# Kernel tuning notes

Hardware: AMD Instinct MI355X
Metric: run time of the kernel (lower is better)

## Reference

```python
import jax, jax.numpy as jnp
import numpy as np
from jax import lax

EPS = 1e-10

def _ln(x, g, b):
    m = x.mean(-1, keepdims=True)
    v = x.var(-1, keepdims=True)
    return (x - m) / jnp.sqrt(v + 1e-5) * g + b

def _gather(t, idx):
    # t: (B, HW, c), idx: (B, HW, d) -> (B, HW, d, c); out[n,i,k,:] = t[n, idx[n,i,k], :]
    return jax.vmap(lambda tn, In: tn[In])(t, idx)

def setup_inputs() -> dict:
    key = jax.random.key(0)
    ks = jax.random.split(key, 20)
    b, v, c, d, h, w, hid, ksz = 2, 2, 128, 64, 64, 64, 256, 5
    hw = h * w
    Bf = b * v  # v_1 == 1 target view per reference view
    std = 0.02
    return {
        'features_mv': jax.random.normal(ks[0], (b, v, c, h, w), jnp.float32),
        'warp_indices': jax.random.randint(ks[1], (Bf, hw, d), 0, hw, jnp.int32),
        'depth_prob': jax.random.uniform(ks[2], (Bf, hw, d), jnp.float32),
        'ln1_g': jnp.ones((c,), jnp.float32), 'ln1_b': jnp.zeros((c,), jnp.float32),
        'wq': jax.random.normal(ks[3], (c, c), jnp.float32) * std, 'bq': jnp.zeros((c,), jnp.float32),
        'wk': jax.random.normal(ks[4], (c, c), jnp.float32) * std, 'bk': jnp.zeros((c,), jnp.float32),
        'wv': jax.random.normal(ks[5], (c, c), jnp.float32) * std, 'bv': jnp.zeros((c,), jnp.float32),
        'k_pe': jax.random.normal(ks[6], (1, 1, d), jnp.float32) * std,
        'v_pe': jax.random.normal(ks[7], (1, 1, d), jnp.float32) * std,
        'rpe': jax.random.normal(ks[8], (1, 1, d), jnp.float32) * std,
        'proj_w': jax.random.normal(ks[9], (c, c), jnp.float32) * std, 'proj_b': jnp.zeros((c,), jnp.float32),
        'ln2_g': jnp.ones((c,), jnp.float32), 'ln2_b': jnp.zeros((c,), jnp.float32),
        'fc1_w': jax.random.normal(ks[10], (c, hid), jnp.float32) * std, 'fc1_b': jnp.zeros((hid,), jnp.float32),
        'dw_w': jax.random.normal(ks[11], (hid, 1, ksz, ksz), jnp.float32) * std, 'dw_b': jnp.zeros((hid,), jnp.float32),
        'fc2_w': jax.random.normal(ks[12], (hid, c), jnp.float32) * std, 'fc2_b': jnp.zeros((c,), jnp.float32),
    }

def reference(features_mv, warp_indices, depth_prob, ln1_g, ln1_b, wq, bq, wk, bk, wv, bv,
              k_pe, v_pe, rpe, proj_w, proj_b, ln2_g, ln2_b, fc1_w, fc1_b, dw_w, dw_b, fc2_w, fc2_b):
    b, v, c, h, w = features_mv.shape
    hw = h * w
    hid = fc1_w.shape[1]
    scale = c ** (-0.5)  # num_heads = 1 -> head_dim = dim

    # (b v) (h w) c
    x = features_mv.reshape(b * v, c, hw).transpose(0, 2, 1)
    shortcut = x
    xn = _ln(x, ln1_g, ln1_b)
    q = xn @ wq + bq
    k = xn @ wk + bk
    vv = xn @ wv + bv

    # nn pairing: v=2, v_1=1 -> each reference view attends the other view
    Q = (q.reshape(b, v, hw, c) * scale).reshape(b * v, hw, c)
    K = k.reshape(b, v, hw, c)[:, ::-1].reshape(b * v, hw, c)
    V = vv.reshape(b, v, hw, c)[:, ::-1].reshape(b * v, hw, c)

    # SMM_QmK: cost[n,i,k] = sum_c Q[n,i,c] * K[n, idx[n,i,k], c]
    Kg = _gather(K, warp_indices)                       # (B, hw, d, c)
    cost = jnp.einsum('bic,bikc->bik', Q, Kg)
    Q_pe = Q.sum(-1, keepdims=True)                     # (B, hw, 1)
    cost = cost + Q_pe * k_pe + rpe                     # broadcast (1,1,d)

    # (Sim_UNet similarity refinement omitted: UNetModel source unavailable; identity here)
    attn = jax.nn.softmax(cost, axis=-1)
    attn = attn * depth_prob
    attn = (attn + EPS) / (attn.sum(-1, keepdims=True) + EPS)

    # SMM_AmV: out[n,i,c] = sum_k attn[n,i,k] * V[n, idx[n,i,k], c]
    Vg = _gather(V, warp_indices)                       # (B, hw, d, c)
    out = jnp.einsum('bik,bikc->bic', attn, Vg)
    out = out + (attn * v_pe).sum(-1, keepdims=True)

    # projection + residual (v_1 == 1 so B == b*v)
    x = shortcut + (out @ proj_w + proj_b)

    # ConvFFN residual branch
    xn2 = _ln(x, ln2_g, ln2_b)
    y = jax.nn.gelu(xn2 @ fc1_w + fc1_b, approximate=False)
    yi = y.transpose(0, 2, 1).reshape(b * v, hid, h, w)
    yc = lax.conv_general_dilated(yi, dw_w, (1, 1), 'SAME', feature_group_count=hid,
                                  dimension_numbers=('NCHW', 'OIHW', 'NCHW'))
    yc = jax.nn.gelu(yc + dw_b[None, :, None, None], approximate=False)
    y = y + yc.reshape(b * v, hid, hw).transpose(0, 2, 1)
    y = y @ fc2_w + fc2_b
    return x + y
```

## Files before the change

kernel.cpp:

```cpp
#include <hip/hip_runtime.h>
#include <math.h>

#define TOK   16384
#define HW    4096
#define C     128
#define D     64
#define HID   256

constexpr float LN_EPS = 1e-5f;
constexpr float EPS_R  = 1e-10f;
constexpr float QSCALE = 0.08838834764831845f;

typedef __attribute__((ext_vector_type(8))) short  bf16x8;
typedef __attribute__((ext_vector_type(4))) float  f32x4;
typedef __attribute__((ext_vector_type(2))) _Float16 half2v;
#define MFMA16(a, b, c) __builtin_amdgcn_mfma_f32_16x16x32_bf16((a), (b), (c), 0, 0, 0)

__device__ __forceinline__ float bflo(unsigned u) { return __uint_as_float(u << 16); }
__device__ __forceinline__ float bfhi(unsigned u) { return __uint_as_float(u & 0xffff0000u); }
__device__ __forceinline__ unsigned short f2bf(float f) {
  unsigned u = __float_as_uint(f);
  unsigned r = (u + 0x7fffu + ((u >> 16) & 1u)) >> 16;
  return (unsigned short)r;
}
__device__ __forceinline__ unsigned short f2h(float f) {
  _Float16 h = (_Float16)f;
  unsigned short r;
  __builtin_memcpy(&r, &h, 2);
  return r;
}
__device__ __forceinline__ float gelu_exact(float x) {
  return 0.5f * x * (1.0f + erff(x * 0.7071067811865476f));
}

union U4H { uint4 v; half2v h[4]; };
union U1H { unsigned v; half2v h; };

#if __has_builtin(__builtin_amdgcn_fdot2)
__device__ __forceinline__ float dot2h(half2v a, half2v b, float c) {
  return __builtin_amdgcn_fdot2(a, b, c, false);
}
#else
__device__ __forceinline__ float dot2h(half2v a, half2v b, float c) {
  return c + (float)a.x * (float)b.x + (float)a.y * (float)b.y;
}
#endif

__global__ __launch_bounds__(256) void k_prep(const float* __restrict__ wq,
    const float* __restrict__ wk, const float* __restrict__ wv,
    const float* __restrict__ pw, const float* __restrict__ f1w,
    const float* __restrict__ f2w, unsigned short* __restrict__ wt) {
  int id = blockIdx.x * 256 + threadIdx.x;
  if (id < 16384) {
    int n = id >> 7, k = id & 127;
    wt[id] = f2bf(wq[k * 128 + n]);
  } else if (id < 32768) {
    int e = id - 16384; int n = e >> 7, k = e & 127;
    wt[id] = f2bf(wk[k * 128 + n]);
  } else if (id < 49152) {
    int e = id - 32768; int n = e >> 7, k = e & 127;
    wt[id] = f2bf(wv[k * 128 + n]);
  } else if (id < 65536) {
    int e = id - 49152; int n = e >> 7, k = e & 127;
    wt[id] = f2bf(pw[k * 128 + n]);
  } else if (id < 98304) {
    int e = id - 65536; int n = e >> 7, k = e & 127;
    wt[id] = f2bf(f1w[k * 256 + n]);
  } else {
    int e = id - 98304; int n = e >> 8, k = e & 255;
    wt[id] = f2bf(f2w[k * 128 + n]);
  }
}

__global__ __launch_bounds__(256) void k_ln1qkv(const float* __restrict__ feat,
    const float* __restrict__ g, const float* __restrict__ b,
    const unsigned short* __restrict__ wt,
    const float* __restrict__ bq, const float* __restrict__ bk,
    const float* __restrict__ bv, unsigned short* __restrict__ qh,
    unsigned short* __restrict__ ksw, unsigned short* __restrict__ vsw) {
  __shared__ float t16[16][C + 1];
  __shared__ unsigned short axn[16 * C];
  int tid = threadIdx.x;
  int lane = tid & 63, wave = tid >> 6;
  int t0 = blockIdx.x * 16;
  int nv = t0 >> 12, i0 = t0 & 4095;
  const float* fb = feat + (size_t)nv * C * HW;
  for (int e = tid; e < 16 * C; e += 256) {
    int ch = e >> 4, ii = e & 15;
    t16[ii][ch] = fb[(size_t)ch * HW + i0 + ii];
  }
  __syncthreads();
  for (int tkn = wave; tkn < 16; tkn += 4) {
    float a0 = t16[tkn][lane];
    float a1 = t16[tkn][lane + 64];
    float s = a0 + a1;
    for (int off = 32; off; off >>= 1) s += __shfl_xor(s, off, 64);
    float mean = s * (1.0f / 128.0f);
    float d0 = a0 - mean, d1 = a1 - mean;
    float v = d0 * d0 + d1 * d1;
    for (int off = 32; off; off >>= 1) v += __shfl_xor(v, off, 64);
    float rstd = rsqrtf(v * (1.0f / 128.0f) + LN_EPS);
    unsigned short x0 = f2bf(d0 * rstd * g[lane] + b[lane]);
    unsigned short x1 = f2bf(d1 * rstd * g[lane + 64] + b[lane + 64]);
    int b0 = (tkn * 256 + lane * 2) ^ ((tkn & 15) << 4);
    int b1 = (tkn * 256 + (lane + 64) * 2) ^ ((tkn & 15) << 4);
    *(unsigned short*)((char*)axn + b0) = x0;
    *(unsigned short*)((char*)axn + b1) = x1;
  }
  __syncthreads();
  int q4 = lane >> 4, m = lane & 15;
  bf16x8 a[4];
  #pragma unroll
  for (int ks = 0; ks < 4; ks++) {
    int boff = (m * 256 + ks * 64 + q4 * 16) ^ (m << 4);
    a[ks] = *(const bf16x8*)((char*)axn + boff);
  }
  int swbase = ((nv ^ 1) << 12) + i0;
  #pragma unroll
  for (int tt = 0; tt < 6; ++tt) {
    int gt = wave * 6 + tt;
    int mat = gt >> 3, ct = gt & 7;
    const unsigned short* bp = wt + mat * 16384 + (size_t)(ct * 16 + m) * C + q4 * 8;
    f32x4 acc = (f32x4){0.f, 0.f, 0.f, 0.f};
    #pragma unroll
    for (int ks = 0; ks < 4; ks++) {
      bf16x8 bfrag = *(const bf16x8*)(bp + ks * 32);
      acc = MFMA16(a[ks], bfrag, acc);
    }
    const float* B = (mat == 0) ? bq : ((mat == 1) ? bk : bv);
    float sc = (mat == 0) ? QSCALE : 1.0f;
    unsigned short* O = (mat == 0) ? qh : ((mat == 1) ? ksw : vsw);
    int base = (mat == 0) ? t0 : swbase;
    int col = ct * 16 + m;
    float bb = B[col];
    #pragma unroll
    for (int reg = 0; reg < 4; reg++) {
      int row = base + q4 * 4 + reg;
      O[(size_t)row * C + col] = f2h((acc[reg] + bb) * sc);
    }
  }
}

__global__ __launch_bounds__(512, 4) void k_attn_proj_fc1(
    const unsigned short* __restrict__ qh, const unsigned short* __restrict__ ksw,
    const unsigned short* __restrict__ vsw, const int* __restrict__ widx,
    const float* __restrict__ dprob, const float* __restrict__ kpe,
    const float* __restrict__ vpe, const float* __restrict__ rpe,
    const unsigned short* __restrict__ wt, const float* __restrict__ pb,
    const float* __restrict__ feat, float* __restrict__ xio,
    const float* __restrict__ g2, const float* __restrict__ b2,
    const float* __restrict__ f1b, unsigned short* __restrict__ y) {
  __shared__ unsigned short axn[16 * C];
  __shared__ float ps1[8][16];
  __shared__ float ps2[8][16];
  int lane = threadIdx.x & 63;
  int wave = threadIdx.x >> 6;
  int bid = blockIdx.x;
  int n = (bid >> 1) & 3;
  int within = ((bid >> 3) << 1) | (bid & 1);
  int T0 = n * HW + within * 16;
  const unsigned short* Kb = ksw + (size_t)n * HW * C;
  const unsigned short* Vb = vsw + (size_t)n * HW * C;
  int gg = lane >> 3, s = lane & 7;
  half2v ones = {(_Float16)1.0f, (_Float16)1.0f};

  for (int tj = 0; tj < 2; ++tj) {
    int token = T0 + wave * 2 + tj;
    int myidx = widx[(size_t)token * D + lane];
    float mydp = dprob[(size_t)token * D + lane];
    half2v qreg[8];
    {
      const unsigned short* qp = qh + (size_t)token * C + s * 16;
      U4H qa, qb2;
      qa.v = *(const uint4*)(qp);
      qb2.v = *(const uint4*)(qp + 8);
      #pragma unroll
      for (int i = 0; i < 4; i++) { qreg[i] = qa.h[i]; qreg[4 + i] = qb2.h[i]; }
    }
    int rowv[8];
    #pragma unroll
    for (int pass = 0; pass < 8; ++pass)
      rowv[pass] = __shfl(myidx, pass * 8 + gg, 64);
    uint4 ka[8], kb[8];
    #pragma unroll
    for (int pass = 0; pass < 8; ++pass) {
      const unsigned short* kr = Kb + (size_t)rowv[pass] * C + s * 16;
      ka[pass] = *(const uint4*)(kr);
      kb[pass] = *(const uint4*)(kr + 8);
    }
    unsigned vv0[32];
    #pragma unroll
    for (int j = 0; j < 32; j++) {
      int row = __builtin_amdgcn_readlane(myidx, j);
      vv0[j] = *(const unsigned*)(Vb + (size_t)row * C + lane * 2);
    }
    float qpe = 0.f;
    #pragma unroll
    for (int i = 0; i < 8; i++) qpe = dot2h(qreg[i], ones, qpe);
    qpe += __shfl_xor(qpe, 1, 64);
    qpe += __shfl_xor(qpe, 2, 64);
    qpe += __shfl_xor(qpe, 4, 64);
    float mycost = 0.f;
    #pragma unroll
    for (int pass = 0; pass < 8; ++pass) {
      U4H ua, ub;
      ua.v = ka[pass]; ub.v = kb[pass];
      float p = 0.f;
      #pragma unroll
      for (int i = 0; i < 4; i++) p = dot2h(ua.h[i], qreg[i], p);
      #pragma unroll
      for (int i = 0; i < 4; i++) p = dot2h(ub.h[i], qreg[4 + i], p);
      p += __shfl_xor(p, 1, 64);
      p += __shfl_xor(p, 2, 64);
      p += __shfl_xor(p, 4, 64);
      float t = __shfl(p, (lane & 7) << 3, 64);
      if (pass == gg) mycost = t;
    }
    mycost += qpe * kpe[lane] + rpe[lane];
    float mx = mycost;
    for (int off = 32; off; off >>= 1) mx = fmaxf(mx, __shfl_xor(mx, off, 64));
    float e = __expf(mycost - mx);
    float ssum = e;
    for (int off = 32; off; off >>= 1) ssum += __shfl_xor(ssum, off, 64);
    float attn = (e / ssum) * mydp;
    float s2 = attn;
    for (int off = 32; off; off >>= 1) s2 += __shfl_xor(s2, off, 64);
    attn = (attn + EPS_R) / (s2 + EPS_R);
    float vpt = attn * vpe[lane];
    for (int off = 32; off; off >>= 1) vpt += __shfl_xor(vpt, off, 64);
    float o0 = vpt, o1 = vpt;
    unsigned att_u = __float_as_uint(attn);
    unsigned vv1[32];
    #pragma unroll
    for (int j = 0; j < 32; j++) {
      int row = __builtin_amdgcn_readlane(myidx, 32 + j);
      vv1[j] = *(const unsigned*)(Vb + (size_t)row * C + lane * 2);
    }
    #pragma unroll
    for (int j = 0; j < 32; j++) {
      float a = __uint_as_float(__builtin_amdgcn_readlane(att_u, j));
      U1H h; h.v = vv0[j];
      o0 += a * (float)h.h.x;
      o1 += a * (float)h.h.y;
    }
    #pragma unroll
    for (int j = 0; j < 32; j++) {
      float a = __uint_as_float(__builtin_amdgcn_readlane(att_u, 32 + j));
      U1H h; h.v = vv1[j];
      o0 += a * (float)h.h.x;
      o1 += a * (float)h.h.y;
    }
    unsigned pk = (unsigned)f2bf(o0) | ((unsigned)f2bf(o1) << 16);
    int row = wave * 2 + tj;
    int boff = (row * 256 + lane * 4) ^ ((row & 15) << 4);
    *(unsigned*)((char*)axn + boff) = pk;
  }
  __syncthreads();

  int q4 = lane >> 4, m = lane & 15;
  bf16x8 a[4];
  #pragma unroll
  for (int ks = 0; ks < 4; ks++) {
    int boff = (m * 256 + ks * 64 + q4 * 16) ^ (m << 4);
    a[ks] = *(const bf16x8*)((char*)axn + boff);
  }
  const unsigned short* Wp = wt + 3 * 16384;
  f32x4 acc = (f32x4){0.f, 0.f, 0.f, 0.f};
  {
    const unsigned short* bp = Wp + (size_t)(wave * 16 + m) * C + q4 * 8;
    #pragma unroll
    for (int ks = 0; ks < 4; ks++) {
      bf16x8 bfrag = *(const bf16x8*)(bp + ks * 32);
      acc = MFMA16(a[ks], bfrag, acc);
    }
  }
  int ibase = (T0 & 4095) + q4 * 4;
  float s1[4], s2b[4];
  {
    int col = wave * 16 + m;
    float bb = pb[col];
    const float* fp = feat + ((size_t)n * C + col) * HW + ibase;
    #pragma unroll
    for (int reg = 0; reg < 4; reg++) {
      float v = acc[reg] + bb + fp[reg];
      acc[reg] = v;
      s1[reg] = v;
      s2b[reg] = v * v;
    }
  }
  #pragma unroll
  for (int reg = 0; reg < 4; reg++) {
    #pragma unroll
    for (int off = 1; off < 16; off <<= 1) {
      s1[reg] += __shfl_xor(s1[reg], off, 64);
      s2b[reg] += __shfl_xor(s2b[reg], off, 64);
    }
  }
  if (m == 0) {
    #pragma unroll
    for (int reg = 0; reg < 4; reg++) {
      ps1[wave][q4 * 4 + reg] = s1[reg];
      ps2[wave][q4 * 4 + reg] = s2b[reg];
    }
  }
  __syncthreads();
  float mean[4], rstd[4];
  #pragma unroll
  for (int reg = 0; reg < 4; reg++) {
    int row = q4 * 4 + reg;
    float t1 = 0.f, t2 = 0.f;
    #pragma unroll
    for (int wv2 = 0; wv2 < 8; wv2++) { t1 += ps1[wv2][row]; t2 += ps2[wv2][row]; }
    mean[reg] = t1 * (1.0f / 128.0f);
    float var = t2 * (1.0f / 128.0f) - mean[reg] * mean[reg];
    rstd[reg] = rsqrtf(var + LN_EPS);
  }
  {
    int col = wave * 16 + m;
    float gc = g2[col], bc = b2[col];
    #pragma unroll
    for (int reg = 0; reg < 4; reg++) {
      int row = q4 * 4 + reg;
      float v = acc[reg];
      xio[(size_t)(T0 + row) * C + col] = v;
      unsigned short xv = f2bf((v - mean[reg]) * rstd[reg] * gc + bc);
      int boff = (row * 256 + col * 2) ^ ((row & 15) << 4);
      *(unsigned short*)((char*)axn + boff) = xv;
    }
  }
  __syncthreads();

  bf16x8 af[4];
  #pragma unroll
  for (int ks = 0; ks < 4; ks++) {
    int boff = (m * 256 + ks * 64 + q4 * 16) ^ (m << 4);
    af[ks] = *(const bf16x8*)((char*)axn + boff);
  }
  const unsigned short* Wf = wt + 65536;
  #pragma unroll
  for (int nt = 0; nt < 2; nt++) {
    int colt = wave * 32 + nt * 16;
    const unsigned short* bp = Wf + (size_t)(colt + m) * C + q4 * 8;
    f32x4 acc2 = (f32x4){0.f, 0.f, 0.f, 0.f};
    #pragma unroll
    for (int ks = 0; ks < 4; ks++) {
      bf16x8 bfrag = *(const bf16x8*)(bp + ks * 32);
      acc2 = MFMA16(af[ks], bfrag, acc2);
    }
    int col = colt + m;
    float bb = f1b[col];
    #pragma unroll
    for (int reg = 0; reg < 4; reg++) {
      int row = T0 + q4 * 4 + reg;
      y[(size_t)row * HID + col] = f2bf(gelu_exact(acc2[reg] + bb));
    }
  }
}

__global__ __launch_bounds__(256) void k_dwconv(const unsigned short* __restrict__ y,
    const float* __restrict__ w, const float* __restrict__ bias,
    unsigned short* __restrict__ ysum) {
  __shared__ float tile[8][401];
  __shared__ float wl[8][25];
  __shared__ float bl[8];
  __shared__ unsigned short outl[256][8];
  int bid = blockIdx.x;
  int tile_id = bid & 15;
  int cb = (bid >> 4) & 31;
  int n = bid >> 9;
  int ty = (tile_id >> 2) * 16, tx = (tile_id & 3) * 16;
  int ch0 = cb * 8;
  int tid = threadIdx.x;
  if (tid < 200) wl[tid / 25][tid % 25] = w[(size_t)(ch0 + tid / 25) * 25 + tid % 25];
  if (tid < 8) bl[tid] = bias[ch0 + tid];
  const unsigned short* yb = y + (size_t)n * HW * HID;
  for (int p = tid; p < 400; p += 256) {
    int py = p / 20, px = p % 20;
    int gy = ty + py - 2, gx = tx + px - 2;
    uint4 v = make_uint4(0u, 0u, 0u, 0u);
    if (gy >= 0 && gy < 64 && gx >= 0 && gx < 64)
      v = *(const uint4*)(yb + (size_t)(gy * 64 + gx) * HID + ch0);
    tile[0][p] = bflo(v.x); tile[1][p] = bfhi(v.x);
    tile[2][p] = bflo(v.y); tile[3][p] = bfhi(v.y);
    tile[4][p] = bflo(v.z); tile[5][p] = bfhi(v.z);
    tile[6][p] = bflo(v.w); tile[7][p] = bfhi(v.w);
  }
  __syncthreads();
  int cc = tid & 7;
  int xx = (tid >> 3) & 15;
  int yg = tid >> 7;
  float wreg[25];
  #pragma unroll
  for (int k = 0; k < 25; k++) wreg[k] = wl[cc][k];
  float bb = bl[cc];
  float win[12][5];
  #pragma unroll
  for (int r = 0; r < 12; r++)
    #pragma unroll
    for (int dx = 0; dx < 5; dx++)
      win[r][dx] = tile[cc][(yg * 8 + r) * 20 + xx + dx];
  #pragma unroll
  for (int j = 0; j < 8; ++j) {
    float acc = 0.f;
    #pragma unroll
    for (int dy = 0; dy < 5; ++dy)
      #pragma unroll
      for (int dx = 0; dx < 5; ++dx)
        acc += wreg[dy * 5 + dx] * win[j + dy][dx];
    float o = win[j + 2][2] + gelu_exact(acc + bb);
    int yy = yg * 8 + j;
    outl[yy * 16 + xx][cc] = f2bf(o);
  }
  __syncthreads();
  {
    int p = tid;
    int yy = p >> 4, xx2 = p & 15;
    uint4 val = *(const uint4*)outl[p];
    *(uint4*)(ysum + (size_t)(n * HW + (ty + yy) * 64 + tx + xx2) * HID + ch0) = val;
  }
}

__global__ __launch_bounds__(256) void k_fc2(const unsigned short* __restrict__ ysum,
    const unsigned short* __restrict__ wt, const float* __restrict__ f2b,
    const float* __restrict__ xio, float* __restrict__ outp) {
  int w = threadIdx.x >> 6, lane = threadIdx.x & 63;
  int q4 = lane >> 4, m = lane & 15;
  int t0 = blockIdx.x * 64 + w * 16;
  int quarter = blockIdx.y;
  const unsigned short* Wt = wt + 98304;
  const unsigned short* ap = ysum + (size_t)(t0 + m) * HID + q4 * 8;
  bf16x8 a[8];
  #pragma unroll
  for (int ks = 0; ks < 8; ks++) a[ks] = *(const bf16x8*)(ap + ks * 32);
  f32x4 acc[2];
  #pragma unroll
  for (int nt = 0; nt < 2; nt++) acc[nt] = (f32x4){0.f, 0.f, 0.f, 0.f};
  #pragma unroll
  for (int nt = 0; nt < 2; nt++) {
    const unsigned short* bp = Wt + (size_t)(quarter * 32 + nt * 16 + m) * HID + q4 * 8;
    #pragma unroll
    for (int ks = 0; ks < 8; ks++) {
      bf16x8 bfrag = *(const bf16x8*)(bp + ks * 32);
      acc[nt] = MFMA16(a[ks], bfrag, acc[nt]);
    }
  }
  #pragma unroll
  for (int nt = 0; nt < 2; nt++) {
    int col = quarter * 32 + nt * 16 + m;
    float bb = f2b[col];
    #pragma unroll
    for (int reg = 0; reg < 4; reg++) {
      int row = t0 + q4 * 4 + reg;
      outp[(size_t)row * C + col] = acc[nt][reg] + bb + xio[(size_t)row * C + col];
    }
  }
}

extern "C" void kernel_launch(void* const* d_in, const int* in_sizes, int n_in,
                              void* d_out, int out_size, void* d_ws, size_t ws_size,
                              hipStream_t stream) {
  (void)in_sizes; (void)n_in; (void)out_size; (void)ws_size;
  const float* feat  = (const float*)d_in[0];
  const int*   widx  = (const int*)d_in[1];
  const float* dprob = (const float*)d_in[2];
  const float* ln1g  = (const float*)d_in[3];
  const float* ln1b  = (const float*)d_in[4];
  const float* wq    = (const float*)d_in[5];
  const float* bq    = (const float*)d_in[6];
  const float* wk    = (const float*)d_in[7];
  const float* bk    = (const float*)d_in[8];
  const float* wv    = (const float*)d_in[9];
  const float* bv    = (const float*)d_in[10];
  const float* kpe   = (const float*)d_in[11];
  const float* vpe   = (const float*)d_in[12];
  const float* rpe   = (const float*)d_in[13];
  const float* pw    = (const float*)d_in[14];
  const float* pb    = (const float*)d_in[15];
  const float* ln2g  = (const float*)d_in[16];
  const float* ln2b  = (const float*)d_in[17];
  const float* f1w   = (const float*)d_in[18];
  const float* f1b   = (const float*)d_in[19];
  const float* dww   = (const float*)d_in[20];
  const float* dwb   = (const float*)d_in[21];
  const float* f2w   = (const float*)d_in[22];
  const float* f2b   = (const float*)d_in[23];

  float* ws = (float*)d_ws;
  const size_t M2 = (size_t)TOK * C;
  float* xio = ws;
  unsigned short* qhb   = (unsigned short*)(ws + M2);
  unsigned short* ksb   = (unsigned short*)(ws + 2 * M2);
  unsigned short* vsb   = (unsigned short*)(ws + 2 * M2 + M2 / 2);
  unsigned short* yb    = (unsigned short*)(ws + 3 * M2);
  unsigned short* ysumb = (unsigned short*)(ws + 4 * M2);
  unsigned short* wtb   = (unsigned short*)(ws + 5 * M2);

  k_prep   <<<512, 256, 0, stream>>>(wq, wk, wv, pw, f1w, f2w, wtb);
  k_ln1qkv <<<1024, 256, 0, stream>>>(feat, ln1g, ln1b, wtb, bq, bk, bv, qhb, ksb, vsb);
  k_attn_proj_fc1<<<1024, 512, 0, stream>>>(qhb, ksb, vsb, widx, dprob, kpe, vpe,
                                            rpe, wtb, pb, feat, xio, ln2g, ln2b,
                                            f1b, yb);
  k_dwconv <<<2048, 256, 0, stream>>>(yb, dww, dwb, ysumb);
  k_fc2    <<<dim3(TOK / 64, 4), 256, 0, stream>>>(ysumb, wtb, f2b, xio, (float*)d_out);
}
```

Baseline: 203.3 us.

## Halve attention block to 4 waves, prefetch second V half, fuse softmax reductions

```diff
diff --git a/kernel.cpp b/kernel.cpp
--- a/kernel.cpp
+++ b/kernel.cpp
@@ -15,6 +15,7 @@
 typedef __attribute__((ext_vector_type(4))) float  f32x4;
 typedef __attribute__((ext_vector_type(2))) _Float16 half2v;
 #define MFMA16(a, b, c) __builtin_amdgcn_mfma_f32_16x16x32_bf16((a), (b), (c), 0, 0, 0)
+#define SBAR() __builtin_amdgcn_sched_barrier(0)
 
 __device__ __forceinline__ float bflo(unsigned u) { return __uint_as_float(u << 16); }
 __device__ __forceinline__ float bfhi(unsigned u) { return __uint_as_float(u & 0xffff0000u); }
@@ -141,7 +142,7 @@
   }
 }
 
-__global__ __launch_bounds__(512, 4) void k_attn_proj_fc1(
+__global__ __launch_bounds__(256, 4) void k_attn_proj_fc1(
     const unsigned short* __restrict__ qh, const unsigned short* __restrict__ ksw,
     const unsigned short* __restrict__ vsw, const int* __restrict__ widx,
     const float* __restrict__ dprob, const float* __restrict__ kpe,
@@ -151,8 +152,8 @@
     const float* __restrict__ g2, const float* __restrict__ b2,
     const float* __restrict__ f1b, unsigned short* __restrict__ y) {
   __shared__ unsigned short axn[16 * C];
-  __shared__ float ps1[8][16];
-  __shared__ float ps2[8][16];
+  __shared__ float ps1[4][16];
+  __shared__ float ps2[4][16];
   int lane = threadIdx.x & 63;
   int wave = threadIdx.x >> 6;
   int bid = blockIdx.x;
@@ -163,9 +164,12 @@
   const unsigned short* Vb = vsw + (size_t)n * HW * C;
   int gg = lane >> 3, s = lane & 7;
   half2v ones = {(_Float16)1.0f, (_Float16)1.0f};
-
-  for (int tj = 0; tj < 2; ++tj) {
-    int token = T0 + wave * 2 + tj;
+  float kpe_l = kpe[lane], rpe_l = rpe[lane], vpe_l = vpe[lane];
+  float Svpe = vpe_l;
+  for (int off = 32; off; off >>= 1) Svpe += __shfl_xor(Svpe, off, 64);
+
+  for (int tj = 0; tj < 4; ++tj) {
+    int token = T0 + wave * 4 + tj;
     int myidx = widx[(size_t)token * D + lane];
     float mydp = dprob[(size_t)token * D + lane];
     half2v qreg[8];
@@ -194,6 +198,7 @@
       int row = __builtin_amdgcn_readlane(myidx, j);
       vv0[j] = *(const unsigned*)(Vb + (size_t)row * C + lane * 2);
     }
+    SBAR();
     float qpe = 0.f;
     #pragma unroll
     for (int i = 0; i < 8; i++) qpe = dot2h(qreg[i], ones, qpe);
@@ -216,26 +221,32 @@
       float t = __shfl(p, (lane & 7) << 3, 64);
       if (pass == gg) mycost = t;
     }
-    mycost += qpe * kpe[lane] + rpe[lane];
+    mycost += qpe * kpe_l + rpe_l;
+    SBAR();
+    unsigned vv1[32];
+    #pragma unroll
+    for (int j = 0; j < 32; j++) {
+      int row = __builtin_amdgcn_readlane(myidx, 32 + j);
+      vv1[j] = *(const unsigned*)(Vb + (size_t)row * C + lane * 2);
+    }
+    SBAR();
     float mx = mycost;
     for (int off = 32; off; off >>= 1) mx = fmaxf(mx, __shfl_xor(mx, off, 64));
     float e = __expf(mycost - mx);
-    float ssum = e;
-    for (int off = 32; off; off >>= 1) ssum += __shfl_xor(ssum, off, 64);
-    float attn = (e / ssum) * mydp;
-    float s2 = attn;
-    for (int off = 32; off; off >>= 1) s2 += __shfl_xor(s2, off, 64);
-    attn = (attn + EPS_R) / (s2 + EPS_R);
-    float vpt = attn * vpe[lane];
-    for (int off = 32; off; off >>= 1) vpt += __shfl_xor(vpt, off, 64);
+    float e1 = e * mydp;
+    float e2 = e1 * vpe_l;
+    float S0 = e, S1 = e1, S2 = e2;
+    for (int off = 32; off; off >>= 1) {
+      S0 += __shfl_xor(S0, off, 64);
+      S1 += __shfl_xor(S1, off, 64);
+      S2 += __shfl_xor(S2, off, 64);
+    }
+    float r = 1.0f / (S1 + EPS_R * S0);
+    float attn = (e1 + EPS_R * S0) * r;
+    float vpt = (S2 + EPS_R * S0 * Svpe) * r;
+    SBAR();
     float o0 = vpt, o1 = vpt;
     unsigned att_u = __float_as_uint(attn);
-    unsigned vv1[32];
-    #pragma unroll
-    for (int j = 0; j < 32; j++) {
-      int row = __builtin_amdgcn_readlane(myidx, 32 + j);
-      vv1[j] = *(const unsigned*)(Vb + (size_t)row * C + lane * 2);
-    }
     #pragma unroll
     for (int j = 0; j < 32; j++) {
       float a = __uint_as_float(__builtin_amdgcn_readlane(att_u, j));
@@ -251,7 +262,7 @@
       o1 += a * (float)h.h.y;
     }
     unsigned pk = (unsigned)f2bf(o0) | ((unsigned)f2bf(o1) << 16);
-    int row = wave * 2 + tj;
+    int row = wave * 4 + tj;
     int boff = (row * 256 + lane * 4) ^ ((row & 15) << 4);
     *(unsigned*)((char*)axn + boff) = pk;
   }
@@ -265,27 +276,32 @@
     a[ks] = *(const bf16x8*)((char*)axn + boff);
   }
   const unsigned short* Wp = wt + 3 * 16384;
-  f32x4 acc = (f32x4){0.f, 0.f, 0.f, 0.f};
-  {
-    const unsigned short* bp = Wp + (size_t)(wave * 16 + m) * C + q4 * 8;
+  f32x4 acc[2];
+  #pragma unroll
+  for (int nt = 0; nt < 2; nt++) acc[nt] = (f32x4){0.f, 0.f, 0.f, 0.f};
+  #pragma unroll
+  for (int nt = 0; nt < 2; nt++) {
+    int colt = wave * 32 + nt * 16;
+    const unsigned short* bp = Wp + (size_t)(colt + m) * C + q4 * 8;
     #pragma unroll
     for (int ks = 0; ks < 4; ks++) {
       bf16x8 bfrag = *(const bf16x8*)(bp + ks * 32);
-      acc = MFMA16(a[ks], bfrag, acc);
+      acc[nt] = MFMA16(a[ks], bfrag, acc[nt]);
     }
   }
   int ibase = (T0 & 4095) + q4 * 4;
-  float s1[4], s2b[4];
-  {
-    int col = wave * 16 + m;
+  float s1[4] = {0.f, 0.f, 0.f, 0.f}, s2b[4] = {0.f, 0.f, 0.f, 0.f};
+  #pragma unroll
+  for (int nt = 0; nt < 2; nt++) {
+    int col = wave * 32 + nt * 16 + m;
     float bb = pb[col];
     const float* fp = feat + ((size_t)n * C + col) * HW + ibase;
     #pragma unroll
     for (int reg = 0; reg < 4; reg++) {
-      float v = acc[reg] + bb + fp[reg];
-      acc[reg] = v;
-      s1[reg] = v;
-      s2b[reg] = v * v;
+      float v = acc[nt][reg] + bb + fp[reg];
+      acc[nt][reg] = v;
+      s1[reg] += v;
+      s2b[reg] += v * v;
     }
   }
   #pragma unroll
@@ -308,20 +324,20 @@
   #pragma unroll
   for (int reg = 0; reg < 4; reg++) {
     int row = q4 * 4 + reg;
-    float t1 = 0.f, t2 = 0.f;
-    #pragma unroll
-    for (int wv2 = 0; wv2 < 8; wv2++) { t1 += ps1[wv2][row]; t2 += ps2[wv2][row]; }
+    float t1 = ps1[0][row] + ps1[1][row] + ps1[2][row] + ps1[3][row];
+    float t2 = ps2[0][row] + ps2[1][row] + ps2[2][row] + ps2[3][row];
     mean[reg] = t1 * (1.0f / 128.0f);
     float var = t2 * (1.0f / 128.0f) - mean[reg] * mean[reg];
     rstd[reg] = rsqrtf(var + LN_EPS);
   }
-  {
-    int col = wave * 16 + m;
+  #pragma unroll
+  for (int nt = 0; nt < 2; nt++) {
+    int col = wave * 32 + nt * 16 + m;
     float gc = g2[col], bc = b2[col];
     #pragma unroll
     for (int reg = 0; reg < 4; reg++) {
       int row = q4 * 4 + reg;
-      float v = acc[reg];
+      float v = acc[nt][reg];
       xio[(size_t)(T0 + row) * C + col] = v;
       unsigned short xv = f2bf((v - mean[reg]) * rstd[reg] * gc + bc);
       int boff = (row * 256 + col * 2) ^ ((row & 15) << 4);
@@ -338,8 +354,8 @@
   }
   const unsigned short* Wf = wt + 65536;
   #pragma unroll
-  for (int nt = 0; nt < 2; nt++) {
-    int colt = wave * 32 + nt * 16;
+  for (int nt = 0; nt < 4; nt++) {
+    int colt = wave * 64 + nt * 16;
     const unsigned short* bp = Wf + (size_t)(colt + m) * C + q4 * 8;
     f32x4 acc2 = (f32x4){0.f, 0.f, 0.f, 0.f};
     #pragma unroll
@@ -497,7 +513,7 @@
 
   k_prep   <<<512, 256, 0, stream>>>(wq, wk, wv, pw, f1w, f2w, wtb);
   k_ln1qkv <<<1024, 256, 0, stream>>>(feat, ln1g, ln1b, wtb, bq, bk, bv, qhb, ksb, vsb);
-  k_attn_proj_fc1<<<1024, 512, 0, stream>>>(qhb, ksb, vsb, widx, dprob, kpe, vpe,
+  k_attn_proj_fc1<<<1024, 256, 0, stream>>>(qhb, ksb, vsb, widx, dprob, kpe, vpe,
                                             rpe, wtb, pb, feat, xio, ln2g, ln2b,
                                             f1b, yb);
   k_dwconv <<<2048, 256, 0, stream>>>(yb, dww, dwb, ysumb);
```

Result: no change. 199.8 us (-1.7%).
